# Optimization experiments

Measured on AMD Instinct MI355X. Metric: run time of the kernel, lower is better.

The kernel has to match this reference:

```python
import jax, jax.numpy as jnp
import numpy as np

U = 64  # LSTM_UNITS

def _lstm(xt, kernel, rec, bias):
    # xt: [B, T, 4U]; keras LSTM gate order i, f, g(c), o
    B = xt.shape[0]
    h0 = jnp.zeros((B, U), xt.dtype)
    c0 = jnp.zeros((B, U), xt.dtype)
    def step(carry, x):
        h, c = carry
        z = x @ kernel + h @ rec + bias  # [B, 4U]
        i, f, g, o = jnp.split(z, 4, axis=-1)
        i = jax.nn.sigmoid(i); f = jax.nn.sigmoid(f)
        g = jnp.tanh(g); o = jax.nn.sigmoid(o)
        c = f * c + i * g
        h = o * jnp.tanh(c)
        return (h, c), h
    _, hs = jax.lax.scan(step, (h0, c0), jnp.swapaxes(xt, 0, 1))
    return jnp.swapaxes(hs, 0, 1)  # [B, T, U]

def setup_inputs() -> dict:
    key = jax.random.key(0)
    ks = jax.random.split(key, 12)
    B, T, P = 8, 100, 1000
    pro_id = jax.random.randint(ks[0], (B, T), 0, P, dtype=jnp.int32)
    label = jax.random.randint(ks[1], (B, T), 0, 2, dtype=jnp.int32)
    X = jax.random.normal(ks[2], (P, 2 * U), jnp.float32)
    cos_X = jax.random.uniform(ks[3], (P, P), jnp.float32)
    trimatrix = jnp.tril(jnp.ones((T, T), jnp.float32))  # causal mask [s, t]
    onehot_table = jax.random.normal(ks[4], (2, 4 * U), jnp.float32)
    s = 0.05
    lstm_kernel = jax.random.normal(ks[5], (4 * U, 4 * U), jnp.float32) * s
    lstm_rec = jax.random.normal(ks[6], (U, 4 * U), jnp.float32) * s
    lstm_bias = jnp.zeros((4 * U,), jnp.float32)
    W1 = jax.random.normal(ks[7], (3 * U, 50), jnp.float32) * s
    b1 = jnp.zeros((50,), jnp.float32)
    W2 = jax.random.normal(ks[8], (50, 1), jnp.float32) * s
    b2 = jnp.zeros((1,), jnp.float32)
    return {"pro_id": pro_id, "label": label, "num_pro": P, "X": X,
            "cos_X": cos_X, "trimatrix": trimatrix, "onehot_table": onehot_table,
            "lstm_kernel": lstm_kernel, "lstm_rec": lstm_rec, "lstm_bias": lstm_bias,
            "W1": W1, "b1": b1, "W2": W2, "b2": b2}

def reference(pro_id, label, num_pro, X, cos_X, trimatrix, onehot_table,
              lstm_kernel, lstm_rec, lstm_bias, W1, b1, W2, b2):
    B, T = pro_id.shape
    # one_hot @ X  ==  gather rows of X
    t_X = jnp.tile(X[pro_id], (1, 1, 2))           # [B, T, 4U]
    label_emb = onehot_table[label]                 # [B, T, 4U]
    xt = t_X * label_emb
    ht = _lstm(xt, lstm_kernel, lstm_rec, lstm_bias)  # [B, T, U]
    a = cos_X[pro_id]                               # [B, T, P] (one_hot @ cos_X)
    # ajhj[b,t,p,u] = sum_s tri[s,t] * a[b,s,p] * ht[b,s,u]  (causal weighted sum)
    ajhj = jnp.einsum('bsp,bsu,st->btpu', a, ht, trimatrix)
    XX = jnp.broadcast_to(X[None, None], (B, T, num_pro, 2 * U))
    hatt = jnp.concatenate([ajhj, XX], axis=-1)     # [B, T, P, 3U]
    r = jax.nn.relu(hatt @ W1 + b1)                 # [B, T, P, 50]
    prediction = r @ W2 + b2                        # [B, T, P, 1]
    return prediction
```

## Files before the change

### kernel.cpp

```cpp
#include <hip/hip_runtime.h>
#include <math.h>

#define BB 8
#define TT 100
#define PP 1000
#define NJ 52
#define GROW 56
#define HSTRIDE 68


__global__ __launch_bounds__(256) void k1_xk(const int* __restrict__ pro_id,
    const int* __restrict__ label, const float* __restrict__ X,
    const float* __restrict__ onehot, const float* __restrict__ kern,
    const float* __restrict__ bias, float* __restrict__ xk)
{
    __shared__ __align__(16) float xt[4][256];
    const int j = threadIdx.x;
    const int r0 = blockIdx.x * 4;
#pragma unroll
    for (int r = 0; r < 4; ++r) {
        int pid = pro_id[r0 + r];
        int lab = label[r0 + r];
        xt[r][j] = X[pid * 128 + (j & 127)] * onehot[lab * 256 + j];
    }
    __syncthreads();
    float acc[4];
    float bj = bias[j];
#pragma unroll
    for (int r = 0; r < 4; ++r) acc[r] = bj;
#pragma unroll 2
    for (int kg = 0; kg < 32; ++kg) {
        const int k0 = kg * 8;
        float kv[8];
#pragma unroll
        for (int i = 0; i < 8; ++i) kv[i] = kern[(k0 + i) * 256 + j];
#pragma unroll
        for (int r = 0; r < 4; ++r) {
            float4 x0 = *(const float4*)&xt[r][k0];
            float4 x1 = *(const float4*)&xt[r][k0 + 4];
            acc[r] += x0.x * kv[0] + x0.y * kv[1] + x0.z * kv[2] + x0.w * kv[3]
                    + x1.x * kv[4] + x1.y * kv[5] + x1.z * kv[6] + x1.w * kv[7];
        }
    }
#pragma unroll
    for (int r = 0; r < 4; ++r) xk[(r0 + r) * 256 + j] = acc[r];
}

__global__ __launch_bounds__(256) void mid(const float* __restrict__ xk,
    const float* __restrict__ rec, const float* __restrict__ W1,
    const float* __restrict__ X, const float* __restrict__ b1,
    float* __restrict__ G, float* __restrict__ XcT)
{
    __shared__ __align__(16) float smem[14720];
    const int tid = threadIdx.x;

    if (blockIdx.x < 8) {
        float* h_all = smem;
        float* w1s   = smem + (TT + 1) * HSTRIDE;
        const int b = blockIdx.x;
        const int l = tid & 63;
        const int w = tid >> 6;
        const int u = (w << 4) | (l & 15);
        const int g = l >> 4;
        const int col = (g << 6) | u;

        for (int idx = tid; idx < 3200; idx += 256) {
            int u2 = idx / 50, jj = idx - u2 * 50;
            w1s[u2 * 52 + jj] = W1[idx];
        }
        float rcol[64];
#pragma unroll
        for (int u2 = 0; u2 < 64; ++u2) rcol[u2] = rec[u2 * 256 + col];

        if (tid < 64) h_all[tid] = 0.f;
        float c = 0.f;
        const float* xkb = xk + b * TT * 256;
        float zc = xkb[col];
        __syncthreads();

        for (int t = 0; t < TT; ++t) {
            float a0 = zc, a1 = 0.f, a2 = 0.f, a3 = 0.f;
            int tn = (t + 1 < TT) ? (t + 1) : (TT - 1);
            zc = xkb[tn * 256 + col];
            const float4* h4p = (const float4*)&h_all[t * HSTRIDE];
#pragma unroll
            for (int m = 0; m < 16; ++m) {
                float4 hv = h4p[m];
                a0 += hv.x * rcol[4 * m + 0];
                a1 += hv.y * rcol[4 * m + 1];
                a2 += hv.z * rcol[4 * m + 2];
                a3 += hv.w * rcol[4 * m + 3];
            }
            float z = (a0 + a1) + (a2 + a3);
            float act;
            if (g == 2) act = 2.f / (1.f + __expf(-2.f * z)) - 1.f;
            else        act = 1.f / (1.f + __expf(-z));
            const int base = l & 15;
            float gi = __shfl(act, base);
            float gf = __shfl(act, base + 16);
            float gg = __shfl(act, base + 32);
            float go = __shfl(act, base + 48);
            c = gf * c + gi * gg;
            float h = go * (2.f / (1.f + __expf(-2.f * c)) - 1.f);
            if (g == 0) h_all[(t + 1) * HSTRIDE + u] = h;
            __syncthreads();
        }

        const int brow0 = b * TT;
        for (int idx = tid; idx < TT * 13; idx += 256) {
            int row = idx / 13;
            int m = idx - row * 13;
            int j = 4 * m;
            const float* hrow = &h_all[(row + 1) * HSTRIDE];
            float ax = 0.f, ay = 0.f, az = 0.f, aw = 0.f;
#pragma unroll
            for (int u4 = 0; u4 < 16; ++u4) {
                float4 hv  = *(const float4*)&hrow[4 * u4];
                float4 w0  = *(const float4*)&w1s[(4 * u4 + 0) * 52 + j];
                float4 w1v = *(const float4*)&w1s[(4 * u4 + 1) * 52 + j];
                float4 w2  = *(const float4*)&w1s[(4 * u4 + 2) * 52 + j];
                float4 w3  = *(const float4*)&w1s[(4 * u4 + 3) * 52 + j];
                ax += hv.x * w0.x + hv.y * w1v.x + hv.z * w2.x + hv.w * w3.x;
                ay += hv.x * w0.y + hv.y * w1v.y + hv.z * w2.y + hv.w * w3.y;
                az += hv.x * w0.z + hv.y * w1v.z + hv.z * w2.z + hv.w * w3.z;
                aw += hv.x * w0.w + hv.y * w1v.w + hv.z * w2.w + hv.w * w3.w;
            }
            if (m == 12) { az = 0.f; aw = 0.f; }
            *(float4*)&G[(brow0 + row) * GROW + j] = make_float4(ax, ay, az, aw);
        }
    } else {
        float* Xs  = smem;
        float* W1T = smem + 8320;
        const int p0 = (blockIdx.x - 8) * 64;
        for (int idx = tid; idx < 6400; idx += 256) {
            int k = idx & 127, jj = idx >> 7;
            W1T[jj * 128 + k] = W1[(64 + k) * 50 + jj];
        }
#pragma unroll
        for (int r = 0; r < 8; ++r) {
            int flat = (tid + 256 * r) * 4;
            int i = flat >> 7;
            int k = flat & 127;
            int p = p0 + i;
            float4 v = make_float4(0.f, 0.f, 0.f, 0.f);
            if (p < PP) v = *(const float4*)&X[p * 128 + k];
            Xs[(k + 0) * 65 + i] = v.x;
            Xs[(k + 1) * 65 + i] = v.y;
            Xs[(k + 2) * 65 + i] = v.z;
            Xs[(k + 3) * 65 + i] = v.w;
        }
        __syncthreads();
        const int ploc = tid & 63;
        const int j0 = tid >> 6;
        float acc[13];
#pragma unroll
        for (int m = 0; m < 13; ++m) {
            int jj = j0 * 13 + m;
            acc[m] = (jj < 50) ? b1[jj] : 0.f;
        }
        for (int k4 = 0; k4 < 32; ++k4) {
            const int k = 4 * k4;
            float x0 = Xs[(k + 0) * 65 + ploc];
            float x1 = Xs[(k + 1) * 65 + ploc];
            float x2 = Xs[(k + 2) * 65 + ploc];
            float x3 = Xs[(k + 3) * 65 + ploc];
#pragma unroll
            for (int m = 0; m < 13; ++m) {
                int jj = j0 * 13 + m;
                if (jj < 50) {
                    float4 w = *(const float4*)&W1T[jj * 128 + k];
                    acc[m] += x0 * w.x + x1 * w.y + x2 * w.z + x3 * w.w;
                }
            }
        }
        int p = p0 + ploc;
        if (p < PP) {
#pragma unroll
            for (int m = 0; m < 13; ++m) {
                int jj = j0 * 13 + m;
                if (jj < 50) XcT[jj * PP + p] = acc[m];
            }
        }
        for (int idx = tid; idx < 6 * 64; idx += 256) {
            int r = 50 + (idx >> 6);
            int pp = p0 + (idx & 63);
            if (pp < PP) XcT[r * PP + pp] = 0.f;
        }
    }
}

__global__ __launch_bounds__(256) void k4_main(const int* __restrict__ pro_id,
    const float* __restrict__ cos_X, const float* __restrict__ XcT,
    const float* __restrict__ G, const float* __restrict__ W2,
    const float* __restrict__ b2, float* __restrict__ out)
{
    __shared__ __align__(16) float Gs[TT * GROW];
    __shared__ float w2s[NJ];
    __shared__ int spid[TT];
    const int b = blockIdx.z;
    const int p = blockIdx.y * 256 + threadIdx.x;
    const int ci = blockIdx.x;
    const int t0 = ci * 7;
    const int t1 = (t0 + 7 < TT) ? (t0 + 7) : TT;
    const bool valid = p < PP;
    const int pc = valid ? p : 0;
    const int tid = threadIdx.x;

    {
        const float4* Gg = (const float4*)(G + b * TT * GROW);
        float4* Gd = (float4*)Gs;
        for (int idx = tid; idx < TT * GROW / 4; idx += 256) Gd[idx] = Gg[idx];
        if (tid < TT) spid[tid] = pro_id[b * TT + tid];
        if (tid < NJ) w2s[tid] = (tid < 50) ? W2[tid] : 0.f;
    }

    float V[NJ];
#pragma unroll
    for (int jj = 0; jj < NJ; ++jj) V[jj] = XcT[jj * PP + pc];
    const float b2v = b2[0];
    __syncthreads();

    const float* cb = cos_X + pc;
    float a0 = cb[spid[99] * PP];
    float a1 = cb[spid[98] * PP];
    float a2 = cb[spid[97] * PP];
    float a3 = cb[spid[96] * PP];

    for (int s = TT - 1; s >= t0; --s) {
        float a = a0; a0 = a1; a1 = a2; a2 = a3;
        int sp = s - 4;
        if (sp < t0) sp = t0;
        a3 = cb[spid[sp] * PP];
        const float4* G4 = (const float4*)&Gs[s * GROW];
#pragma unroll
        for (int jv = 0; jv < 13; ++jv) {
            float4 gv = G4[jv];
            V[4 * jv + 0] += a * gv.x;
            V[4 * jv + 1] += a * gv.y;
            V[4 * jv + 2] += a * gv.z;
            V[4 * jv + 3] += a * gv.w;
        }
        if (s < t1) {
            float acc = b2v;
#pragma unroll
            for (int jv = 0; jv < 13; ++jv) {
                float4 wv = *(const float4*)&w2s[4 * jv];
                acc += wv.x * fmaxf(V[4 * jv + 0], 0.f)
                     + wv.y * fmaxf(V[4 * jv + 1], 0.f)
                     + wv.z * fmaxf(V[4 * jv + 2], 0.f)
                     + wv.w * fmaxf(V[4 * jv + 3], 0.f);
            }
            if (valid) out[(b * TT + s) * PP + p] = acc;
        }
    }
}

extern "C" void kernel_launch(void* const* d_in, const int* in_sizes, int n_in,
                              void* d_out, int out_size, void* d_ws, size_t ws_size,
                              hipStream_t stream)
{
    const int* pro_id  = (const int*)d_in[0];
    const int* label   = (const int*)d_in[1];
    const float* X     = (const float*)d_in[3];
    const float* cos_X = (const float*)d_in[4];
    const float* onehot = (const float*)d_in[6];
    const float* lk    = (const float*)d_in[7];
    const float* lr    = (const float*)d_in[8];
    const float* lb    = (const float*)d_in[9];
    const float* W1    = (const float*)d_in[10];
    const float* b1    = (const float*)d_in[11];
    const float* W2    = (const float*)d_in[12];
    const float* b2    = (const float*)d_in[13];

    float* ws  = (float*)d_ws;
    float* xk  = ws;
    float* XcT = ws + 204800;
    float* G   = ws + 260800;
    float* out = (float*)d_out;

    hipLaunchKernelGGL(k1_xk,  dim3(200),      dim3(256), 0, stream,
                       pro_id, label, X, onehot, lk, lb, xk);
    hipLaunchKernelGGL(mid,    dim3(24),       dim3(256), 0, stream,
                       xk, lr, W1, X, b1, G, XcT);
    hipLaunchKernelGGL(k4_main,dim3(15, 4, 8), dim3(256), 0, stream,
                       pro_id, cos_X, XcT, G, W2, b2, out);
}
```

Before: 210.2 us.

## Run LSTM recurrence in a single wavefront without block barriers

```diff
diff --git a/kernel.cpp b/kernel.cpp
--- a/kernel.cpp
+++ b/kernel.cpp
@@ -14,39 +14,42 @@
     const float* __restrict__ onehot, const float* __restrict__ kern,
     const float* __restrict__ bias, float* __restrict__ xk)
 {
-    __shared__ __align__(16) float xt[4][256];
+    __shared__ __align__(16) float xt[2][256];
     const int j = threadIdx.x;
-    const int r0 = blockIdx.x * 4;
-#pragma unroll
-    for (int r = 0; r < 4; ++r) {
+    const int r0 = blockIdx.x * 2;
+#pragma unroll
+    for (int r = 0; r < 2; ++r) {
         int pid = pro_id[r0 + r];
         int lab = label[r0 + r];
         xt[r][j] = X[pid * 128 + (j & 127)] * onehot[lab * 256 + j];
     }
     __syncthreads();
-    float acc[4];
-    float bj = bias[j];
-#pragma unroll
-    for (int r = 0; r < 4; ++r) acc[r] = bj;
-#pragma unroll 2
+    float acc0 = bias[j], acc1 = acc0;
+    float kc[8];
+#pragma unroll
+    for (int i = 0; i < 8; ++i) kc[i] = kern[i * 256 + j];
     for (int kg = 0; kg < 32; ++kg) {
+        float kn[8];
+        const int kgn = (kg < 31) ? kg + 1 : 31;
+#pragma unroll
+        for (int i = 0; i < 8; ++i) kn[i] = kern[(kgn * 8 + i) * 256 + j];
         const int k0 = kg * 8;
-        float kv[8];
-#pragma unroll
-        for (int i = 0; i < 8; ++i) kv[i] = kern[(k0 + i) * 256 + j];
-#pragma unroll
-        for (int r = 0; r < 4; ++r) {
-            float4 x0 = *(const float4*)&xt[r][k0];
-            float4 x1 = *(const float4*)&xt[r][k0 + 4];
-            acc[r] += x0.x * kv[0] + x0.y * kv[1] + x0.z * kv[2] + x0.w * kv[3]
-                    + x1.x * kv[4] + x1.y * kv[5] + x1.z * kv[6] + x1.w * kv[7];
-        }
-    }
-#pragma unroll
-    for (int r = 0; r < 4; ++r) xk[(r0 + r) * 256 + j] = acc[r];
+        float4 xa0 = *(const float4*)&xt[0][k0];
+        float4 xa1 = *(const float4*)&xt[0][k0 + 4];
+        float4 xb0 = *(const float4*)&xt[1][k0];
+        float4 xb1 = *(const float4*)&xt[1][k0 + 4];
+        acc0 += xa0.x * kc[0] + xa0.y * kc[1] + xa0.z * kc[2] + xa0.w * kc[3]
+              + xa1.x * kc[4] + xa1.y * kc[5] + xa1.z * kc[6] + xa1.w * kc[7];
+        acc1 += xb0.x * kc[0] + xb0.y * kc[1] + xb0.z * kc[2] + xb0.w * kc[3]
+              + xb1.x * kc[4] + xb1.y * kc[5] + xb1.z * kc[6] + xb1.w * kc[7];
+#pragma unroll
+        for (int i = 0; i < 8; ++i) kc[i] = kn[i];
+    }
+    xk[(r0 + 0) * 256 + j] = acc0;
+    xk[(r0 + 1) * 256 + j] = acc1;
 }
 
-__global__ __launch_bounds__(256) void mid(const float* __restrict__ xk,
+__global__ __launch_bounds__(256, 1) void mid(const float* __restrict__ xk,
     const float* __restrict__ rec, const float* __restrict__ W1,
     const float* __restrict__ X, const float* __restrict__ b1,
     float* __restrict__ G, float* __restrict__ XcT)
@@ -58,53 +61,64 @@
         float* h_all = smem;
         float* w1s   = smem + (TT + 1) * HSTRIDE;
         const int b = blockIdx.x;
-        const int l = tid & 63;
-        const int w = tid >> 6;
-        const int u = (w << 4) | (l & 15);
-        const int g = l >> 4;
-        const int col = (g << 6) | u;
 
         for (int idx = tid; idx < 3200; idx += 256) {
             int u2 = idx / 50, jj = idx - u2 * 50;
             w1s[u2 * 52 + jj] = W1[idx];
         }
-        float rcol[64];
-#pragma unroll
-        for (int u2 = 0; u2 < 64; ++u2) rcol[u2] = rec[u2 * 256 + col];
-
         if (tid < 64) h_all[tid] = 0.f;
-        float c = 0.f;
-        const float* xkb = xk + b * TT * 256;
-        float zc = xkb[col];
         __syncthreads();
 
-        for (int t = 0; t < TT; ++t) {
-            float a0 = zc, a1 = 0.f, a2 = 0.f, a3 = 0.f;
-            int tn = (t + 1 < TT) ? (t + 1) : (TT - 1);
-            zc = xkb[tn * 256 + col];
-            const float4* h4p = (const float4*)&h_all[t * HSTRIDE];
-#pragma unroll
-            for (int m = 0; m < 16; ++m) {
-                float4 hv = h4p[m];
-                a0 += hv.x * rcol[4 * m + 0];
-                a1 += hv.y * rcol[4 * m + 1];
-                a2 += hv.z * rcol[4 * m + 2];
-                a3 += hv.w * rcol[4 * m + 3];
-            }
-            float z = (a0 + a1) + (a2 + a3);
-            float act;
-            if (g == 2) act = 2.f / (1.f + __expf(-2.f * z)) - 1.f;
-            else        act = 1.f / (1.f + __expf(-z));
-            const int base = l & 15;
-            float gi = __shfl(act, base);
-            float gf = __shfl(act, base + 16);
-            float gg = __shfl(act, base + 32);
-            float go = __shfl(act, base + 48);
-            c = gf * c + gi * gg;
-            float h = go * (2.f / (1.f + __expf(-2.f * c)) - 1.f);
-            if (g == 0) h_all[(t + 1) * HSTRIDE + u] = h;
-            __syncthreads();
-        }
+        if (tid < 64) {
+            const int u = tid;
+            const float* xkb = xk + b * TT * 256;
+            float2 rif[64], rgo[64];
+#pragma unroll
+            for (int u2 = 0; u2 < 64; ++u2) {
+                const float* rr = rec + u2 * 256;
+                rif[u2] = make_float2(rr[u], rr[64 + u]);
+                rgo[u2] = make_float2(rr[128 + u], rr[192 + u]);
+            }
+            float c = 0.f;
+            float2 aif = make_float2(xkb[u], xkb[64 + u]);
+            float2 ago = make_float2(xkb[128 + u], xkb[192 + u]);
+            float2 bif = make_float2(xkb[256 + u], xkb[256 + 64 + u]);
+            float2 bgo = make_float2(xkb[256 + 128 + u], xkb[256 + 192 + u]);
+            float2 cif = make_float2(xkb[512 + u], xkb[512 + 64 + u]);
+            float2 cgo = make_float2(xkb[512 + 128 + u], xkb[512 + 192 + u]);
+
+            for (int t = 0; t < TT; ++t) {
+                float2 zif = aif, zgo = ago;
+                aif = bif; ago = bgo; bif = cif; bgo = cgo;
+                int tn = (t + 3 < TT) ? t + 3 : TT - 1;
+                const float* xp = xkb + tn * 256;
+                cif = make_float2(xp[u], xp[64 + u]);
+                cgo = make_float2(xp[128 + u], xp[192 + u]);
+
+                const float4* h4p = (const float4*)&h_all[t * HSTRIDE];
+#pragma unroll
+                for (int m = 0; m < 16; ++m) {
+                    float4 h4 = h4p[m];
+                    zif.x += h4.x * rif[4 * m + 0].x; zif.y += h4.x * rif[4 * m + 0].y;
+                    zgo.x += h4.x * rgo[4 * m + 0].x; zgo.y += h4.x * rgo[4 * m + 0].y;
+                    zif.x += h4.y * rif[4 * m + 1].x; zif.y += h4.y * rif[4 * m + 1].y;
+                    zgo.x += h4.y * rgo[4 * m + 1].x; zgo.y += h4.y * rgo[4 * m + 1].y;
+                    zif.x += h4.z * rif[4 * m + 2].x; zif.y += h4.z * rif[4 * m + 2].y;
+                    zgo.x += h4.z * rgo[4 * m + 2].x; zgo.y += h4.z * rgo[4 * m + 2].y;
+                    zif.x += h4.w * rif[4 * m + 3].x; zif.y += h4.w * rif[4 * m + 3].y;
+                    zgo.x += h4.w * rgo[4 * m + 3].x; zgo.y += h4.w * rgo[4 * m + 3].y;
+                }
+                float gi = 1.f / (1.f + __expf(-zif.x));
+                float gf = 1.f / (1.f + __expf(-zif.y));
+                float gg = 2.f / (1.f + __expf(-2.f * zgo.x)) - 1.f;
+                float go = 1.f / (1.f + __expf(-zgo.y));
+                c = gf * c + gi * gg;
+                float h = go * (2.f / (1.f + __expf(-2.f * c)) - 1.f);
+                h_all[(t + 1) * HSTRIDE + u] = h;
+                __builtin_amdgcn_s_waitcnt(0xc07f);
+            }
+        }
+        __syncthreads();
 
         const int brow0 = b * TT;
         for (int idx = tid; idx < TT * 13; idx += 256) {
@@ -278,7 +292,7 @@
     float* G   = ws + 260800;
     float* out = (float*)d_out;
 
-    hipLaunchKernelGGL(k1_xk,  dim3(200),      dim3(256), 0, stream,
+    hipLaunchKernelGGL(k1_xk,  dim3(400),      dim3(256), 0, stream,
                        pro_id, label, X, onehot, lk, lb, xk);
     hipLaunchKernelGGL(mid,    dim3(24),       dim3(256), 0, stream,
                        xk, lr, W1, X, b1, G, XcT);
```

New measurement: 263.3 us. +25.3%, slower.
